# Kernel optimization log

Hardware: AMD Instinct MI355X
Metric: run time of the kernel (lower is better)

Reference implementation:

```python
import jax, jax.numpy as jnp
import numpy as np

K = 20000   # know_num
I = 50000   # item_num
D = 128     # emb_dim
N = K + I   # nodes in exer+know graphs (exercises first)
E1 = 320000 # edges in directed knowledge graph
E2 = 640000 # edges in each exer<->know graph


def setup_inputs() -> dict:
    key = jax.random.key(0)
    ks = jax.random.split(key, 20)
    s = 1.0 / np.sqrt(D)
    s2 = 1.0 / np.sqrt(2 * D)
    return {
        'kn_emb': jax.random.normal(ks[0], (K, D), jnp.float32),
        'exer_emb': jax.random.normal(ks[1], (I, D), jnp.float32),
        # GAT params: W is fc.weight.T ([in,out]); a is attn_fc.weight flattened ([2D])
        'W_dir': jax.random.normal(ks[2], (D, D), jnp.float32) * s,
        'a_dir': jax.random.normal(ks[3], (2 * D,), jnp.float32) * s2,
        'W_ke': jax.random.normal(ks[4], (D, D), jnp.float32) * s,
        'a_ke': jax.random.normal(ks[5], (2 * D,), jnp.float32) * s2,
        'W_ek': jax.random.normal(ks[6], (D, D), jnp.float32) * s,
        'a_ek': jax.random.normal(ks[7], (2 * D,), jnp.float32) * s2,
        # relation attention MLP: Linear(D,D)+bias, Tanh, Linear(D,1,no bias)
        'rel_W1': jax.random.normal(ks[8], (D, D), jnp.float32) * s,
        'rel_b1': jax.random.normal(ks[9], (D,), jnp.float32) * s,
        'rel_w2': jax.random.normal(ks[10], (D,), jnp.float32) * s,
        # edge lists (src, dst)
        'directed_src': jax.random.randint(ks[11], (E1,), 0, K),
        'directed_dst': jax.random.randint(ks[12], (E1,), 0, K),
        'ke_src': jax.random.randint(ks[13], (E2,), 0, N),
        'ke_dst': jax.random.randint(ks[14], (E2,), 0, N),
        'ek_src': jax.random.randint(ks[15], (E2,), 0, N),
        'ek_dst': jax.random.randint(ks[16], (E2,), 0, N),
    }


def _gat(h, W, a, src, dst, n):
    # GraphLayer: z = fc(h); e = leaky_relu(attn_fc([z_src; z_dst]));
    # alpha = softmax_e over dst; h_out = sum alpha * z_src
    z = h @ W                                   # [n_in, D]
    # split attn vector: cat([z_src,z_dst]) @ a == z_src@a[:D] + z_dst@a[D:]
    s_src = z @ a[:D]                           # [n_in]
    s_dst = z @ a[D:]                           # [n_in]
    e = jax.nn.leaky_relu(s_src[src] + s_dst[dst], 0.01)  # [E]
    m = jax.ops.segment_max(e, dst, num_segments=n)
    ex = jnp.exp(e - m[dst])
    den = jax.ops.segment_sum(ex, dst, num_segments=n)
    alpha = ex / den[dst]                       # segment softmax over in-edges
    return jax.ops.segment_sum(alpha[:, None] * z[src], dst, num_segments=n)


def reference(kn_emb, exer_emb, W_dir, a_dir, W_ke, a_ke, W_ek, a_ek,
              rel_W1, rel_b1, rel_w2,
              directed_src, directed_dst, ke_src, ke_dst, ek_src, ek_dst):
    A = _gat(kn_emb, W_dir, a_dir, directed_src, directed_dst, K)      # [K,D]
    ek = jnp.concatenate([exer_emb, kn_emb], axis=0)                   # [N,D]
    B = _gat(ek, W_ke, a_ke, ke_src, ke_dst, N)[I:]                    # [K,D]
    Cfull = _gat(ek, W_ek, a_ek, ek_src, ek_dst, N)                    # [N,D]
    s1 = jnp.tanh(A @ rel_W1 + rel_b1) @ rel_w2                        # [K]
    s2 = jnp.tanh(B @ rel_W1 + rel_b1) @ rel_w2                        # [K]
    score = jax.nn.softmax(jnp.stack([s1, s2], axis=1), axis=1)        # [K,2]
    kn_out = score[:, 0:1] * A + score[:, 1:2] * B                     # [K,D]
    exer_out = Cfull[:I]                                               # [I,D]
    return (kn_out, exer_out)
```

## Files before the change

### kernel.cpp

```cpp
#include <hip/hip_runtime.h>
#include <math.h>

#define KN   20000
#define IN_  50000
#define DD   128
#define NN   70000
#define E1N  320000
#define E2N  640000

#define GB0  313
#define GB1  1094
#define GB2  1094
#define GTILES 2501

#define GROUPS 313
#define MGRID  (GROUPS*13)
#define CNT_CHUNKS 1563

#define CAP   64
#define LCAP  6

typedef _Float16 f16x8 __attribute__((ext_vector_type(8)));
typedef float floatx4 __attribute__((ext_vector_type(4)));

__device__ __forceinline__ unsigned f2bf(float x) {
  unsigned u = __float_as_uint(x);
  return (u + 0x7FFFu + ((u >> 16) & 1u)) >> 16;
}
__device__ __forceinline__ unsigned packbf(float a, float b) {
  return f2bf(a) | (f2bf(b) << 16);
}
__device__ __forceinline__ float bf_lo(unsigned u) { return __uint_as_float(u << 16); }
__device__ __forceinline__ float bf_hi(unsigned u) { return __uint_as_float(u & 0xFFFF0000u); }

__device__ __forceinline__ float ftanh(float x) {
  x = fminf(15.f, fmaxf(-15.f, x));
  float t = __expf(2.f * x);
  return (t - 1.f) / (t + 1.f);
}

__global__ __launch_bounds__(256) void prep(
    const float* __restrict__ W0, const float* __restrict__ W1,
    const float* __restrict__ W2, const float* __restrict__ W3,
    short* __restrict__ wfr)
{
  int b = blockIdx.x;
  int wsel = b >> 3;
  const float* W = (wsel == 0) ? W0 : (wsel == 1) ? W1 : (wsel == 2) ? W2 : W3;
  int fi = (b & 7) * 256 + threadIdx.x;
  int l = fi & 63, chunk = (fi >> 6) & 3, t = fi >> 8;
  int col = t * 16 + (l & 15);
  int kbase = chunk * 32 + (l >> 4) * 8;
  f16x8 hv;
#pragma unroll
  for (int j = 0; j < 8; ++j) hv[j] = (_Float16)W[(kbase + j) * 128 + col];
  ((f16x8*)(wfr + wsel * 16384))[fi] = hv;
}

__global__ __launch_bounds__(256, 4) void gemm3_insert(
    const float* __restrict__ kn, const float* __restrict__ ex,
    const short* __restrict__ wfr,
    const float* __restrict__ a_dir, const float* __restrict__ a_ke, const float* __restrict__ a_ek,
    unsigned* __restrict__ zb_dir, unsigned* __restrict__ zb_ke, unsigned* __restrict__ zb_ek,
    float* __restrict__ sds, float* __restrict__ sdd,
    float* __restrict__ sks, float* __restrict__ skd,
    float* __restrict__ ses, float* __restrict__ sed,
    const int* __restrict__ dsrc, const int* __restrict__ ddst,
    const int* __restrict__ kesrc, const int* __restrict__ kedst,
    const int* __restrict__ eksrc, const int* __restrict__ ekdst,
    int* __restrict__ cur_dir, int* __restrict__ cur_ke, int* __restrict__ cur_ek,
    int* __restrict__ epp_dir, int* __restrict__ epp_ke, int* __restrict__ epp_ek)
{
  __shared__ short sW[16384];
  const int g = blockIdx.x / 13;
  const int r = blockIdx.x % 13;
  const int tid = threadIdx.x;

  if (r >= 8) {
    int cidx = g * 5 + (r - 8);
    if (cidx >= CNT_CHUNKS) return;
    int t = cidx * 256 + tid;
    if (t < 80000) {
      int e0 = t * 4;
      int4 s4 = *(const int4*)(dsrc + e0);
      int4 d4 = *(const int4*)(ddst + e0);
      int p;
      p = atomicAdd(&cur_dir[d4.x], 1); if (p < CAP) epp_dir[(d4.x << LCAP) + p] = s4.x;
      p = atomicAdd(&cur_dir[d4.y], 1); if (p < CAP) epp_dir[(d4.y << LCAP) + p] = s4.y;
      p = atomicAdd(&cur_dir[d4.z], 1); if (p < CAP) epp_dir[(d4.z << LCAP) + p] = s4.z;
      p = atomicAdd(&cur_dir[d4.w], 1); if (p < CAP) epp_dir[(d4.w << LCAP) + p] = s4.w;
    } else if (t < 240000) {
      int e0 = (t - 80000) * 4;
      int4 s4 = *(const int4*)(kesrc + e0);
      int4 d4 = *(const int4*)(kedst + e0);
      int p;
      if (d4.x >= IN_) { p = atomicAdd(&cur_ke[d4.x - IN_], 1); if (p < CAP) epp_ke[((d4.x - IN_) << LCAP) + p] = s4.x; }
      if (d4.y >= IN_) { p = atomicAdd(&cur_ke[d4.y - IN_], 1); if (p < CAP) epp_ke[((d4.y - IN_) << LCAP) + p] = s4.y; }
      if (d4.z >= IN_) { p = atomicAdd(&cur_ke[d4.z - IN_], 1); if (p < CAP) epp_ke[((d4.z - IN_) << LCAP) + p] = s4.z; }
      if (d4.w >= IN_) { p = atomicAdd(&cur_ke[d4.w - IN_], 1); if (p < CAP) epp_ke[((d4.w - IN_) << LCAP) + p] = s4.w; }
    } else if (t < 400000) {
      int e0 = (t - 240000) * 4;
      int4 s4 = *(const int4*)(eksrc + e0);
      int4 d4 = *(const int4*)(ekdst + e0);
      int p;
      if (d4.x < IN_) { p = atomicAdd(&cur_ek[d4.x], 1); if (p < CAP) epp_ek[(d4.x << LCAP) + p] = s4.x; }
      if (d4.y < IN_) { p = atomicAdd(&cur_ek[d4.y], 1); if (p < CAP) epp_ek[(d4.y << LCAP) + p] = s4.y; }
      if (d4.z < IN_) { p = atomicAdd(&cur_ek[d4.z], 1); if (p < CAP) epp_ek[(d4.z << LCAP) + p] = s4.z; }
      if (d4.w < IN_) { p = atomicAdd(&cur_ek[d4.w], 1); if (p < CAP) epp_ek[(d4.w << LCAP) + p] = s4.w; }
    }
    return;
  }

  const int bid = g * 8 + r;
  if (bid >= GTILES) return;

  const float *h1, *h2, *avec;
  unsigned* zb;
  float *ssrc, *sdst;
  const short* wf;
  int split, rows, tile;
  if (bid < GB0) {
    tile = bid; rows = KN; split = KN; h1 = kn; h2 = kn;
    wf = wfr; avec = a_dir; zb = zb_dir; ssrc = sds; sdst = sdd;
  } else if (bid < GB0 + GB1) {
    tile = bid - GB0; rows = NN; split = IN_; h1 = ex; h2 = kn;
    wf = wfr + 16384; avec = a_ke; zb = zb_ke; ssrc = sks; sdst = skd;
  } else {
    tile = bid - GB0 - GB1; rows = NN; split = IN_; h1 = ex; h2 = kn;
    wf = wfr + 32768; avec = a_ek; zb = zb_ek; ssrc = ses; sdst = sed;
  }

  {
    const int4* gs = (const int4*)wf;
    int4* ls = (int4*)sW;
#pragma unroll
    for (int it = 0; it < 8; ++it) ls[it * 256 + tid] = gs[it * 256 + tid];
  }
  __syncthreads();

  const int lane = tid & 63;
  const int wv = tid >> 6;
  const int q = lane >> 4;
  const int m = lane & 15;
  const int rr = tile * 64 + wv * 16 + m;
  const int rc = (rr < rows) ? rr : (rows - 1);
  const float* hp = (rc < split) ? (h1 + (size_t)rc * 128)
                                 : (h2 + (size_t)(rc - split) * 128);

  floatx4 acc[8];
#pragma unroll
  for (int t = 0; t < 8; ++t) { acc[t][0]=0.f; acc[t][1]=0.f; acc[t][2]=0.f; acc[t][3]=0.f; }

#pragma unroll
  for (int chunk = 0; chunk < 4; ++chunk) {
    float4 v0 = *(const float4*)(hp + chunk * 32 + q * 8);
    float4 v1 = *(const float4*)(hp + chunk * 32 + q * 8 + 4);
    float vs[8] = {v0.x, v0.y, v0.z, v0.w, v1.x, v1.y, v1.z, v1.w};
    f16x8 ahi, alo;
#pragma unroll
    for (int j = 0; j < 8; ++j) {
      _Float16 h = (_Float16)vs[j];
      ahi[j] = h;
      alo[j] = (_Float16)(vs[j] - (float)h);
    }
#pragma unroll
    for (int t = 0; t < 8; ++t) {
      f16x8 bh = ((const f16x8*)sW)[(t * 4 + chunk) * 64 + lane];
      acc[t] = __builtin_amdgcn_mfma_f32_16x16x32_f16(bh, ahi, acc[t], 0, 0, 0);
      acc[t] = __builtin_amdgcn_mfma_f32_16x16x32_f16(bh, alo, acc[t], 0, 0, 0);
    }
  }

  if (rr < rows) {
    unsigned* zrow = zb + (size_t)rr * 64;
#pragma unroll
    for (int t = 0; t < 8; ++t) {
      uint2 pk;
      pk.x = packbf(acc[t][0], acc[t][1]);
      pk.y = packbf(acc[t][2], acc[t][3]);
      *(uint2*)(zrow + t * 8 + q * 2) = pk;
    }
  }
  float d1 = 0.f, d2 = 0.f;
#pragma unroll
  for (int t = 0; t < 8; ++t) {
    float4 wa = *(const float4*)(avec + t * 16 + q * 4);
    float4 wb = *(const float4*)(avec + 128 + t * 16 + q * 4);
    d1 += acc[t][0] * wa.x + acc[t][1] * wa.y + acc[t][2] * wa.z + acc[t][3] * wa.w;
    d2 += acc[t][0] * wb.x + acc[t][1] * wb.y + acc[t][2] * wb.z + acc[t][3] * wb.w;
  }
  d1 += __shfl_xor(d1, 16, 64); d1 += __shfl_xor(d1, 32, 64);
  d2 += __shfl_xor(d2, 16, 64); d2 += __shfl_xor(d2, 32, 64);
  if (q == 0 && rr < rows) { ssrc[rr] = d1; sdst[rr] = d2; }
}

__global__ __launch_bounds__(256) void gat_gather(
    const int* __restrict__ cur_dir, const int* __restrict__ epp_dir,
    const float* __restrict__ sds, const float* __restrict__ sdd,
    const unsigned* __restrict__ zb_dir, float* __restrict__ A,
    const int* __restrict__ cur_ke, const int* __restrict__ epp_ke,
    const float* __restrict__ sks, const float* __restrict__ skd,
    const unsigned* __restrict__ zb_ke, float* __restrict__ Bm,
    const int* __restrict__ cur_ek, const int* __restrict__ epp_ek,
    const float* __restrict__ ses, const float* __restrict__ sed,
    const unsigned* __restrict__ zb_ek, float* __restrict__ Cout)
{
  int gw = (blockIdx.x * 256 + threadIdx.x) >> 6;
  int lane = threadIdx.x & 63;
  int h = lane >> 5;
  int ln31 = lane & 31;
  int gh = (lane >> 4) & 1;
  int gl = lane & 15;

  const int *cur, *ep;
  const float *ss, *sD;
  const unsigned* zb;
  float* out;
  int s0, nodeoff;
  if (gw < 10000)      { s0 = 2 * gw;           cur = cur_dir; ep = epp_dir; ss = sds; sD = sdd; zb = zb_dir; out = A;    nodeoff = 0; }
  else if (gw < 20000) { s0 = 2 * (gw - 10000); cur = cur_ke;  ep = epp_ke;  ss = sks; sD = skd; zb = zb_ke;  out = Bm;   nodeoff = IN_; }
  else                 { s0 = 2 * (gw - 20000); cur = cur_ek;  ep = epp_ek;  ss = ses; sD = sed; zb = zb_ek;  out = Cout; nodeoff = 0; }

  int2 cc = *(const int2*)(cur + s0);
  int cnt = h ? cc.y : cc.x;
  cnt = (cnt < CAP) ? cnt : CAP;
  int b = (s0 + h) << LCAP;
  float sd = sD[s0 + h + nodeoff];
  int lim = (cnt < 32) ? cnt : 32;

  int   src_l = 0;
  float w_l   = 0.f;
  if (ln31 < lim) {
    int s = ep[b + ln31];
    src_l = s;
    float x = ss[s] + sd;
    x = (x > 0.f) ? x : 0.01f * x;
    w_l = __expf(x);
  }

  float den = w_l;
  den += __shfl_xor(den, 1, 64);
  den += __shfl_xor(den, 2, 64);
  den += __shfl_xor(den, 4, 64);
  den += __shfl_xor(den, 8, 64);
  den += __shfl_xor(den, 16, 64);

  float av[8];
#pragma unroll
  for (int k = 0; k < 8; ++k) av[k] = 0.f;

  for (int j0 = 0; j0 < lim; j0 += 8) {
    int base = h * 32 + j0 + gh * 4;
    int   s1 = __shfl(src_l, base + 0, 64); float w1 = __shfl(w_l, base + 0, 64);
    int   s2 = __shfl(src_l, base + 1, 64); float w2 = __shfl(w_l, base + 1, 64);
    int   s3 = __shfl(src_l, base + 2, 64); float w3 = __shfl(w_l, base + 2, 64);
    int   s4 = __shfl(src_l, base + 3, 64); float w4 = __shfl(w_l, base + 3, 64);
    uint4 za = *(const uint4*)(zb + (size_t)s1 * 64 + gl * 4);
    uint4 zc = *(const uint4*)(zb + (size_t)s2 * 64 + gl * 4);
    uint4 ze = *(const uint4*)(zb + (size_t)s3 * 64 + gl * 4);
    uint4 zg = *(const uint4*)(zb + (size_t)s4 * 64 + gl * 4);
    av[0] += w1 * bf_lo(za.x); av[1] += w1 * bf_hi(za.x);
    av[2] += w1 * bf_lo(za.y); av[3] += w1 * bf_hi(za.y);
    av[4] += w1 * bf_lo(za.z); av[5] += w1 * bf_hi(za.z);
    av[6] += w1 * bf_lo(za.w); av[7] += w1 * bf_hi(za.w);
    av[0] += w2 * bf_lo(zc.x); av[1] += w2 * bf_hi(zc.x);
    av[2] += w2 * bf_lo(zc.y); av[3] += w2 * bf_hi(zc.y);
    av[4] += w2 * bf_lo(zc.z); av[5] += w2 * bf_hi(zc.z);
    av[6] += w2 * bf_lo(zc.w); av[7] += w2 * bf_hi(zc.w);
    av[0] += w3 * bf_lo(ze.x); av[1] += w3 * bf_hi(ze.x);
    av[2] += w3 * bf_lo(ze.y); av[3] += w3 * bf_hi(ze.y);
    av[4] += w3 * bf_lo(ze.z); av[5] += w3 * bf_hi(ze.z);
    av[6] += w3 * bf_lo(ze.w); av[7] += w3 * bf_hi(ze.w);
    av[0] += w4 * bf_lo(zg.x); av[1] += w4 * bf_hi(zg.x);
    av[2] += w4 * bf_lo(zg.y); av[3] += w4 * bf_hi(zg.y);
    av[4] += w4 * bf_lo(zg.z); av[5] += w4 * bf_hi(zg.z);
    av[6] += w4 * bf_lo(zg.w); av[7] += w4 * bf_hi(zg.w);
  }

  if (cnt > 32) {
    float dtail = 0.f;
    int e = b + cnt;
    for (int i = b + 32 + gh; i < e; i += 2) {
      int sx = ep[i];
      float x1 = ss[sx] + sd;
      x1 = (x1 > 0.f) ? x1 : 0.01f * x1;
      float w1 = __expf(x1);
      uint4 za = *(const uint4*)(zb + (size_t)sx * 64 + gl * 4);
      dtail += w1;
      av[0] += w1 * bf_lo(za.x); av[1] += w1 * bf_hi(za.x);
      av[2] += w1 * bf_lo(za.y); av[3] += w1 * bf_hi(za.y);
      av[4] += w1 * bf_lo(za.z); av[5] += w1 * bf_hi(za.z);
      av[6] += w1 * bf_lo(za.w); av[7] += w1 * bf_hi(za.w);
    }
    den += dtail + __shfl_xor(dtail, 16, 64);
  }

#pragma unroll
  for (int k = 0; k < 8; ++k) av[k] += __shfl_xor(av[k], 16, 64);

  if (cnt > 0) {
    float inv = 1.f / den;
#pragma unroll
    for (int k = 0; k < 8; ++k) av[k] *= inv;
  }

  if (gh == 0) {
    int seg = s0 + h;
    float* op = out + (size_t)seg * 128 + gl * 8;
    *(float4*)op       = make_float4(av[0], av[1], av[2], av[3]);
    *(float4*)(op + 4) = make_float4(av[4], av[5], av[6], av[7]);
  }
}

__global__ __launch_bounds__(256, 2) void relgemm_combine(
    const float* __restrict__ Am, const float* __restrict__ Bm,
    const short* __restrict__ wfr_rel,
    const float* __restrict__ rb1, const float* __restrict__ rw2,
    float* __restrict__ out)
{
  __shared__ short sW[16384];
  const int tid = threadIdx.x;
  {
    const int4* gs = (const int4*)wfr_rel;
    int4* ls = (int4*)sW;
#pragma unroll
    for (int it = 0; it < 8; ++it) ls[it * 256 + tid] = gs[it * 256 + tid];
  }
  __syncthreads();

  const int lane = tid & 63;
  const int wv = tid >> 6;
  const int q = lane >> 4;
  const int m = lane & 15;
  const int r = blockIdx.x * 64 + wv * 16 + m;
  const int rc = (r < KN) ? r : (KN - 1);
  const float* hA = Am + (size_t)rc * 128;
  const float* hB = Bm + (size_t)rc * 128;

  floatx4 accA[8], accB[8];
#pragma unroll
  for (int t = 0; t < 8; ++t) {
    accA[t][0]=0.f; accA[t][1]=0.f; accA[t][2]=0.f; accA[t][3]=0.f;
    accB[t][0]=0.f; accB[t][1]=0.f; accB[t][2]=0.f; accB[t][3]=0.f;
  }

#pragma unroll
  for (int chunk = 0; chunk < 4; ++chunk) {
    float4 a0 = *(const float4*)(hA + chunk * 32 + q * 8);
    float4 a1 = *(const float4*)(hA + chunk * 32 + q * 8 + 4);
    float4 b0 = *(const float4*)(hB + chunk * 32 + q * 8);
    float4 b1 = *(const float4*)(hB + chunk * 32 + q * 8 + 4);
    float as[8] = {a0.x, a0.y, a0.z, a0.w, a1.x, a1.y, a1.z, a1.w};
    float bs[8] = {b0.x, b0.y, b0.z, b0.w, b1.x, b1.y, b1.z, b1.w};
    f16x8 ahiA, aloA, ahiB, aloB;
#pragma unroll
    for (int j = 0; j < 8; ++j) {
      _Float16 ha = (_Float16)as[j];
      ahiA[j] = ha; aloA[j] = (_Float16)(as[j] - (float)ha);
      _Float16 hb = (_Float16)bs[j];
      ahiB[j] = hb; aloB[j] = (_Float16)(bs[j] - (float)hb);
    }
#pragma unroll
    for (int t = 0; t < 8; ++t) {
      f16x8 bh = ((const f16x8*)sW)[(t * 4 + chunk) * 64 + lane];
      accA[t] = __builtin_amdgcn_mfma_f32_16x16x32_f16(bh, ahiA, accA[t], 0, 0, 0);
      accA[t] = __builtin_amdgcn_mfma_f32_16x16x32_f16(bh, aloA, accA[t], 0, 0, 0);
      accB[t] = __builtin_amdgcn_mfma_f32_16x16x32_f16(bh, ahiB, accB[t], 0, 0, 0);
      accB[t] = __builtin_amdgcn_mfma_f32_16x16x32_f16(bh, aloB, accB[t], 0, 0, 0);
    }
  }

  float p1 = 0.f, p2 = 0.f;
#pragma unroll
  for (int t = 0; t < 8; ++t) {
    float4 bb = *(const float4*)(rb1 + t * 16 + q * 4);
    float4 ww = *(const float4*)(rw2 + t * 16 + q * 4);
    p1 += ftanh(accA[t][0] + bb.x) * ww.x + ftanh(accA[t][1] + bb.y) * ww.y +
          ftanh(accA[t][2] + bb.z) * ww.z + ftanh(accA[t][3] + bb.w) * ww.w;
    p2 += ftanh(accB[t][0] + bb.x) * ww.x + ftanh(accB[t][1] + bb.y) * ww.y +
          ftanh(accB[t][2] + bb.z) * ww.z + ftanh(accB[t][3] + bb.w) * ww.w;
  }
  p1 += __shfl_xor(p1, 16, 64); p1 += __shfl_xor(p1, 32, 64);
  p2 += __shfl_xor(p2, 16, 64); p2 += __shfl_xor(p2, 32, 64);

  float mx = fmaxf(p1, p2);
  float e1 = __expf(p1 - mx), e2 = __expf(p2 - mx);
  float al = e1 / (e1 + e2), be = e2 / (e1 + e2);

  if (r < KN) {
#pragma unroll
    for (int t = 0; t < 8; ++t) {
      int col = t * 16 + q * 4;
      float4 avv = *(const float4*)(Am + (size_t)r * 128 + col);
      float4 bvv = *(const float4*)(Bm + (size_t)r * 128 + col);
      *(float4*)(out + (size_t)r * 128 + col) =
          make_float4(al * avv.x + be * bvv.x, al * avv.y + be * bvv.y,
                      al * avv.z + be * bvv.z, al * avv.w + be * bvv.w);
    }
  }
}

extern "C" void kernel_launch(void* const* d_in, const int* in_sizes, int n_in,
                              void* d_out, int out_size, void* d_ws, size_t ws_size,
                              hipStream_t stream) {
  const float* kn    = (const float*)d_in[0];
  const float* ex    = (const float*)d_in[1];
  const float* W_dir = (const float*)d_in[2];
  const float* a_dir = (const float*)d_in[3];
  const float* W_ke  = (const float*)d_in[4];
  const float* a_ke  = (const float*)d_in[5];
  const float* W_ek  = (const float*)d_in[6];
  const float* a_ek  = (const float*)d_in[7];
  const float* rW1   = (const float*)d_in[8];
  const float* rb1   = (const float*)d_in[9];
  const float* rw2   = (const float*)d_in[10];
  const int* dsrc    = (const int*)d_in[11];
  const int* ddst    = (const int*)d_in[12];
  const int* kesrc   = (const int*)d_in[13];
  const int* kedst   = (const int*)d_in[14];
  const int* eksrc   = (const int*)d_in[15];
  const int* ekdst   = (const int*)d_in[16];
  float* out = (float*)d_out;

  char* p = (char*)d_ws;
  auto alloc = [&](size_t bytes) {
    char* r = p;
    p += (bytes + 255) & ~(size_t)255;
    return r;
  };
  unsigned* zb_dir = (unsigned*)alloc((size_t)KN * 64 * 4);
  unsigned* zb_ke  = (unsigned*)alloc((size_t)NN * 64 * 4);
  unsigned* zb_ek  = (unsigned*)alloc((size_t)NN * 64 * 4);
  float* Am    = (float*)alloc((size_t)KN * 128 * 4);
  float* Bmat  = (float*)alloc((size_t)KN * 128 * 4);
  short* wfr   = (short*)alloc((size_t)4 * 16384 * 2);
  float* sds = (float*)alloc(KN * 4);
  float* sdd = (float*)alloc(KN * 4);
  float* sks = (float*)alloc(NN * 4);
  float* skd = (float*)alloc(NN * 4);
  float* ses = (float*)alloc(NN * 4);
  float* sed = (float*)alloc(NN * 4);
  int* cur = (int*)alloc((size_t)(KN + KN + IN_) * 4);
  int* cur_dir = cur;
  int* cur_ke  = cur + KN;
  int* cur_ek  = cur + 2 * KN;
  int* epp_dir = (int*)alloc((size_t)KN * CAP * 4);
  int* epp_ke  = (int*)alloc((size_t)KN * CAP * 4);
  int* epp_ek  = (int*)alloc((size_t)IN_ * CAP * 4);

  hipMemsetAsync(cur, 0, (size_t)(KN + KN + IN_) * 4, stream);

  prep<<<32, 256, 0, stream>>>(W_dir, W_ke, W_ek, rW1, wfr);

  gemm3_insert<<<MGRID, 256, 0, stream>>>(
      kn, ex, wfr, a_dir, a_ke, a_ek,
      zb_dir, zb_ke, zb_ek,
      sds, sdd, sks, skd, ses, sed,
      dsrc, ddst, kesrc, kedst, eksrc, ekdst,
      cur_dir, cur_ke, cur_ek,
      epp_dir, epp_ke, epp_ek);

  gat_gather<<<11250, 256, 0, stream>>>(
      cur_dir, epp_dir, sds, sdd, zb_dir, Am,
      cur_ke,  epp_ke,  sks, skd, zb_ke,  Bmat,
      cur_ek,  epp_ek,  ses, sed, zb_ek,  out + (size_t)KN * 128);

  relgemm_combine<<<313, 256, 0, stream>>>(Am, Bmat, wfr + 3 * 16384, rb1, rw2, out);
}
```

Before: 231.1 us.

## Fuse ke/ek projection GEMMs per tile and drop weight prep kernel

Removes the separate prep kernel. Each block now converts the fp32 weight matrix to the fp16 MFMA fragment layout directly in shared memory. The ke and ek projections share the same input rows, so one block loads and splits each row tile into hi/lo fp16 once and runs both GEMMs. This halves input reads for those graphs and cuts a launch. The cost is strided fp32 weight loads and conversion repeated in every block. The grid interleaving with edge-insertion blocks is also rebalanced (9 GEMM + 10 count blocks per group).

```diff
diff --git a/kernel.cpp b/kernel.cpp
--- a/kernel.cpp
+++ b/kernel.cpp
@@ -10,11 +10,10 @@
 
 #define GB0  313
 #define GB1  1094
-#define GB2  1094
-#define GTILES 2501
-
-#define GROUPS 313
-#define MGRID  (GROUPS*13)
+#define GTILES 1407
+
+#define GROUPS 157
+#define MGRID  (GROUPS*19)
 #define CNT_CHUNKS 1563
 
 #define CAP   64
@@ -39,27 +38,24 @@
   return (t - 1.f) / (t + 1.f);
 }
 
-__global__ __launch_bounds__(256) void prep(
-    const float* __restrict__ W0, const float* __restrict__ W1,
-    const float* __restrict__ W2, const float* __restrict__ W3,
-    short* __restrict__ wfr)
-{
-  int b = blockIdx.x;
-  int wsel = b >> 3;
-  const float* W = (wsel == 0) ? W0 : (wsel == 1) ? W1 : (wsel == 2) ? W2 : W3;
-  int fi = (b & 7) * 256 + threadIdx.x;
-  int l = fi & 63, chunk = (fi >> 6) & 3, t = fi >> 8;
-  int col = t * 16 + (l & 15);
-  int kbase = chunk * 32 + (l >> 4) * 8;
-  f16x8 hv;
-#pragma unroll
-  for (int j = 0; j < 8; ++j) hv[j] = (_Float16)W[(kbase + j) * 128 + col];
-  ((f16x8*)(wfr + wsel * 16384))[fi] = hv;
+__device__ __forceinline__ void stage_w(const float* __restrict__ W,
+                                        short* __restrict__ sW, int tid) {
+#pragma unroll
+  for (int it = 0; it < 8; ++it) {
+    int fi = it * 256 + tid;
+    int l = fi & 63, chunk = (fi >> 6) & 3, t = fi >> 8;
+    int col = t * 16 + (l & 15);
+    int kbase = chunk * 32 + (l >> 4) * 8;
+    f16x8 hv;
+#pragma unroll
+    for (int j = 0; j < 8; ++j) hv[j] = (_Float16)W[(kbase + j) * 128 + col];
+    ((f16x8*)sW)[fi] = hv;
+  }
 }
 
 __global__ __launch_bounds__(256, 4) void gemm3_insert(
     const float* __restrict__ kn, const float* __restrict__ ex,
-    const short* __restrict__ wfr,
+    const float* __restrict__ W_dir, const float* __restrict__ W_ke, const float* __restrict__ W_ek,
     const float* __restrict__ a_dir, const float* __restrict__ a_ke, const float* __restrict__ a_ek,
     unsigned* __restrict__ zb_dir, unsigned* __restrict__ zb_ke, unsigned* __restrict__ zb_ek,
     float* __restrict__ sds, float* __restrict__ sdd,
@@ -72,12 +68,12 @@
     int* __restrict__ epp_dir, int* __restrict__ epp_ke, int* __restrict__ epp_ek)
 {
   __shared__ short sW[16384];
-  const int g = blockIdx.x / 13;
-  const int r = blockIdx.x % 13;
+  const int g = blockIdx.x / 19;
+  const int r = blockIdx.x % 19;
   const int tid = threadIdx.x;
 
-  if (r >= 8) {
-    int cidx = g * 5 + (r - 8);
+  if (r >= 9) {
+    int cidx = g * 10 + (r - 9);
     if (cidx >= CNT_CHUNKS) return;
     int t = cidx * 256 + tid;
     if (t < 80000) {
@@ -111,87 +107,169 @@
     return;
   }
 
-  const int bid = g * 8 + r;
+  const int bid = g * 9 + r;
   if (bid >= GTILES) return;
-
-  const float *h1, *h2, *avec;
-  unsigned* zb;
-  float *ssrc, *sdst;
-  const short* wf;
-  int split, rows, tile;
-  if (bid < GB0) {
-    tile = bid; rows = KN; split = KN; h1 = kn; h2 = kn;
-    wf = wfr; avec = a_dir; zb = zb_dir; ssrc = sds; sdst = sdd;
-  } else if (bid < GB0 + GB1) {
-    tile = bid - GB0; rows = NN; split = IN_; h1 = ex; h2 = kn;
-    wf = wfr + 16384; avec = a_ke; zb = zb_ke; ssrc = sks; sdst = skd;
-  } else {
-    tile = bid - GB0 - GB1; rows = NN; split = IN_; h1 = ex; h2 = kn;
-    wf = wfr + 32768; avec = a_ek; zb = zb_ek; ssrc = ses; sdst = sed;
-  }
-
-  {
-    const int4* gs = (const int4*)wf;
-    int4* ls = (int4*)sW;
-#pragma unroll
-    for (int it = 0; it < 8; ++it) ls[it * 256 + tid] = gs[it * 256 + tid];
-  }
-  __syncthreads();
 
   const int lane = tid & 63;
   const int wv = tid >> 6;
   const int q = lane >> 4;
   const int m = lane & 15;
-  const int rr = tile * 64 + wv * 16 + m;
-  const int rc = (rr < rows) ? rr : (rows - 1);
-  const float* hp = (rc < split) ? (h1 + (size_t)rc * 128)
-                                 : (h2 + (size_t)(rc - split) * 128);
-
-  floatx4 acc[8];
-#pragma unroll
-  for (int t = 0; t < 8; ++t) { acc[t][0]=0.f; acc[t][1]=0.f; acc[t][2]=0.f; acc[t][3]=0.f; }
-
-#pragma unroll
-  for (int chunk = 0; chunk < 4; ++chunk) {
-    float4 v0 = *(const float4*)(hp + chunk * 32 + q * 8);
-    float4 v1 = *(const float4*)(hp + chunk * 32 + q * 8 + 4);
-    float vs[8] = {v0.x, v0.y, v0.z, v0.w, v1.x, v1.y, v1.z, v1.w};
-    f16x8 ahi, alo;
-#pragma unroll
-    for (int j = 0; j < 8; ++j) {
-      _Float16 h = (_Float16)vs[j];
-      ahi[j] = h;
-      alo[j] = (_Float16)(vs[j] - (float)h);
-    }
+
+  if (bid < GB0) {
+    const int rr = bid * 64 + wv * 16 + m;
+    const int rc = (rr < KN) ? rr : (KN - 1);
+    const float* hp = kn + (size_t)rc * 128;
+
+    stage_w(W_dir, sW, tid);
+    __syncthreads();
+
+    floatx4 acc[8];
+#pragma unroll
+    for (int t = 0; t < 8; ++t) { acc[t][0]=0.f; acc[t][1]=0.f; acc[t][2]=0.f; acc[t][3]=0.f; }
+
+#pragma unroll
+    for (int chunk = 0; chunk < 4; ++chunk) {
+      float4 v0 = *(const float4*)(hp + chunk * 32 + q * 8);
+      float4 v1 = *(const float4*)(hp + chunk * 32 + q * 8 + 4);
+      float vs[8] = {v0.x, v0.y, v0.z, v0.w, v1.x, v1.y, v1.z, v1.w};
+      f16x8 ahi, alo;
+#pragma unroll
+      for (int j = 0; j < 8; ++j) {
+        _Float16 h = (_Float16)vs[j];
+        ahi[j] = h;
+        alo[j] = (_Float16)(vs[j] - (float)h);
+      }
+#pragma unroll
+      for (int t = 0; t < 8; ++t) {
+        f16x8 bh = ((const f16x8*)sW)[(t * 4 + chunk) * 64 + lane];
+        acc[t] = __builtin_amdgcn_mfma_f32_16x16x32_f16(bh, ahi, acc[t], 0, 0, 0);
+        acc[t] = __builtin_amdgcn_mfma_f32_16x16x32_f16(bh, alo, acc[t], 0, 0, 0);
+      }
+    }
+
+    if (rr < KN) {
+      unsigned* zrow = zb_dir + (size_t)rr * 64;
+#pragma unroll
+      for (int t = 0; t < 8; ++t) {
+        uint2 pk;
+        pk.x = packbf(acc[t][0], acc[t][1]);
+        pk.y = packbf(acc[t][2], acc[t][3]);
+        *(uint2*)(zrow + t * 8 + q * 2) = pk;
+      }
+    }
+    float d1 = 0.f, d2 = 0.f;
 #pragma unroll
     for (int t = 0; t < 8; ++t) {
-      f16x8 bh = ((const f16x8*)sW)[(t * 4 + chunk) * 64 + lane];
-      acc[t] = __builtin_amdgcn_mfma_f32_16x16x32_f16(bh, ahi, acc[t], 0, 0, 0);
-      acc[t] = __builtin_amdgcn_mfma_f32_16x16x32_f16(bh, alo, acc[t], 0, 0, 0);
-    }
-  }
-
-  if (rr < rows) {
-    unsigned* zrow = zb + (size_t)rr * 64;
-#pragma unroll
-    for (int t = 0; t < 8; ++t) {
-      uint2 pk;
-      pk.x = packbf(acc[t][0], acc[t][1]);
-      pk.y = packbf(acc[t][2], acc[t][3]);
-      *(uint2*)(zrow + t * 8 + q * 2) = pk;
-    }
-  }
-  float d1 = 0.f, d2 = 0.f;
-#pragma unroll
-  for (int t = 0; t < 8; ++t) {
-    float4 wa = *(const float4*)(avec + t * 16 + q * 4);
-    float4 wb = *(const float4*)(avec + 128 + t * 16 + q * 4);
-    d1 += acc[t][0] * wa.x + acc[t][1] * wa.y + acc[t][2] * wa.z + acc[t][3] * wa.w;
-    d2 += acc[t][0] * wb.x + acc[t][1] * wb.y + acc[t][2] * wb.z + acc[t][3] * wb.w;
-  }
-  d1 += __shfl_xor(d1, 16, 64); d1 += __shfl_xor(d1, 32, 64);
-  d2 += __shfl_xor(d2, 16, 64); d2 += __shfl_xor(d2, 32, 64);
-  if (q == 0 && rr < rows) { ssrc[rr] = d1; sdst[rr] = d2; }
+      float4 wa = *(const float4*)(a_dir + t * 16 + q * 4);
+      float4 wb = *(const float4*)(a_dir + 128 + t * 16 + q * 4);
+      d1 += acc[t][0] * wa.x + acc[t][1] * wa.y + acc[t][2] * wa.z + acc[t][3] * wa.w;
+      d2 += acc[t][0] * wb.x + acc[t][1] * wb.y + acc[t][2] * wb.z + acc[t][3] * wb.w;
+    }
+    d1 += __shfl_xor(d1, 16, 64); d1 += __shfl_xor(d1, 32, 64);
+    d2 += __shfl_xor(d2, 16, 64); d2 += __shfl_xor(d2, 32, 64);
+    if (q == 0 && rr < KN) { sds[rr] = d1; sdd[rr] = d2; }
+    return;
+  }
+
+  {
+    const int tile = bid - GB0;
+    const int rr = tile * 64 + wv * 16 + m;
+    const int rc = (rr < NN) ? rr : (NN - 1);
+    const float* hp = (rc < IN_) ? (ex + (size_t)rc * 128)
+                                 : (kn + (size_t)(rc - IN_) * 128);
+
+    f16x8 fhi[4], flo[4];
+#pragma unroll
+    for (int chunk = 0; chunk < 4; ++chunk) {
+      float4 v0 = *(const float4*)(hp + chunk * 32 + q * 8);
+      float4 v1 = *(const float4*)(hp + chunk * 32 + q * 8 + 4);
+      float vs[8] = {v0.x, v0.y, v0.z, v0.w, v1.x, v1.y, v1.z, v1.w};
+#pragma unroll
+      for (int j = 0; j < 8; ++j) {
+        _Float16 h = (_Float16)vs[j];
+        fhi[chunk][j] = h;
+        flo[chunk][j] = (_Float16)(vs[j] - (float)h);
+      }
+    }
+
+    stage_w(W_ke, sW, tid);
+    __syncthreads();
+
+    floatx4 acc[8];
+#pragma unroll
+    for (int t = 0; t < 8; ++t) { acc[t][0]=0.f; acc[t][1]=0.f; acc[t][2]=0.f; acc[t][3]=0.f; }
+#pragma unroll
+    for (int chunk = 0; chunk < 4; ++chunk) {
+#pragma unroll
+      for (int t = 0; t < 8; ++t) {
+        f16x8 bh = ((const f16x8*)sW)[(t * 4 + chunk) * 64 + lane];
+        acc[t] = __builtin_amdgcn_mfma_f32_16x16x32_f16(bh, fhi[chunk], acc[t], 0, 0, 0);
+        acc[t] = __builtin_amdgcn_mfma_f32_16x16x32_f16(bh, flo[chunk], acc[t], 0, 0, 0);
+      }
+    }
+    if (rr < NN) {
+      unsigned* zrow = zb_ke + (size_t)rr * 64;
+#pragma unroll
+      for (int t = 0; t < 8; ++t) {
+        uint2 pk;
+        pk.x = packbf(acc[t][0], acc[t][1]);
+        pk.y = packbf(acc[t][2], acc[t][3]);
+        *(uint2*)(zrow + t * 8 + q * 2) = pk;
+      }
+    }
+    {
+      float d1 = 0.f, d2 = 0.f;
+#pragma unroll
+      for (int t = 0; t < 8; ++t) {
+        float4 wa = *(const float4*)(a_ke + t * 16 + q * 4);
+        float4 wb = *(const float4*)(a_ke + 128 + t * 16 + q * 4);
+        d1 += acc[t][0] * wa.x + acc[t][1] * wa.y + acc[t][2] * wa.z + acc[t][3] * wa.w;
+        d2 += acc[t][0] * wb.x + acc[t][1] * wb.y + acc[t][2] * wb.z + acc[t][3] * wb.w;
+      }
+      d1 += __shfl_xor(d1, 16, 64); d1 += __shfl_xor(d1, 32, 64);
+      d2 += __shfl_xor(d2, 16, 64); d2 += __shfl_xor(d2, 32, 64);
+      if (q == 0 && rr < NN) { sks[rr] = d1; skd[rr] = d2; }
+    }
+
+    __syncthreads();
+    stage_w(W_ek, sW, tid);
+    __syncthreads();
+
+#pragma unroll
+    for (int t = 0; t < 8; ++t) { acc[t][0]=0.f; acc[t][1]=0.f; acc[t][2]=0.f; acc[t][3]=0.f; }
+#pragma unroll
+    for (int chunk = 0; chunk < 4; ++chunk) {
+#pragma unroll
+      for (int t = 0; t < 8; ++t) {
+        f16x8 bh = ((const f16x8*)sW)[(t * 4 + chunk) * 64 + lane];
+        acc[t] = __builtin_amdgcn_mfma_f32_16x16x32_f16(bh, fhi[chunk], acc[t], 0, 0, 0);
+        acc[t] = __builtin_amdgcn_mfma_f32_16x16x32_f16(bh, flo[chunk], acc[t], 0, 0, 0);
+      }
+    }
+    if (rr < NN) {
+      unsigned* zrow = zb_ek + (size_t)rr * 64;
+#pragma unroll
+      for (int t = 0; t < 8; ++t) {
+        uint2 pk;
+        pk.x = packbf(acc[t][0], acc[t][1]);
+        pk.y = packbf(acc[t][2], acc[t][3]);
+        *(uint2*)(zrow + t * 8 + q * 2) = pk;
+      }
+    }
+    {
+      float d1 = 0.f, d2 = 0.f;
+#pragma unroll
+      for (int t = 0; t < 8; ++t) {
+        float4 wa = *(const float4*)(a_ek + t * 16 + q * 4);
+        float4 wb = *(const float4*)(a_ek + 128 + t * 16 + q * 4);
+        d1 += acc[t][0] * wa.x + acc[t][1] * wa.y + acc[t][2] * wa.z + acc[t][3] * wa.w;
+        d2 += acc[t][0] * wb.x + acc[t][1] * wb.y + acc[t][2] * wb.z + acc[t][3] * wb.w;
+      }
+      d1 += __shfl_xor(d1, 16, 64); d1 += __shfl_xor(d1, 32, 64);
+      d2 += __shfl_xor(d2, 16, 64); d2 += __shfl_xor(d2, 32, 64);
+      if (q == 0 && rr < NN) { ses[rr] = d1; sed[rr] = d2; }
+    }
+  }
 }
 
 __global__ __launch_bounds__(256) void gat_gather(
@@ -314,18 +392,13 @@
 
 __global__ __launch_bounds__(256, 2) void relgemm_combine(
     const float* __restrict__ Am, const float* __restrict__ Bm,
-    const short* __restrict__ wfr_rel,
+    const float* __restrict__ rW1,
     const float* __restrict__ rb1, const float* __restrict__ rw2,
     float* __restrict__ out)
 {
   __shared__ short sW[16384];
   const int tid = threadIdx.x;
-  {
-    const int4* gs = (const int4*)wfr_rel;
-    int4* ls = (int4*)sW;
-#pragma unroll
-    for (int it = 0; it < 8; ++it) ls[it * 256 + tid] = gs[it * 256 + tid];
-  }
+  stage_w(rW1, sW, tid);
   __syncthreads();
 
   const int lane = tid & 63;
@@ -433,7 +506,6 @@
   unsigned* zb_ek  = (unsigned*)alloc((size_t)NN * 64 * 4);
   float* Am    = (float*)alloc((size_t)KN * 128 * 4);
   float* Bmat  = (float*)alloc((size_t)KN * 128 * 4);
-  short* wfr   = (short*)alloc((size_t)4 * 16384 * 2);
   float* sds = (float*)alloc(KN * 4);
   float* sdd = (float*)alloc(KN * 4);
   float* sks = (float*)alloc(NN * 4);
@@ -450,10 +522,8 @@
 
   hipMemsetAsync(cur, 0, (size_t)(KN + KN + IN_) * 4, stream);
 
-  prep<<<32, 256, 0, stream>>>(W_dir, W_ke, W_ek, rW1, wfr);
-
   gemm3_insert<<<MGRID, 256, 0, stream>>>(
-      kn, ex, wfr, a_dir, a_ke, a_ek,
+      kn, ex, W_dir, W_ke, W_ek, a_dir, a_ke, a_ek,
       zb_dir, zb_ke, zb_ek,
       sds, sdd, sks, skd, ses, sed,
       dsrc, ddst, kesrc, kedst, eksrc, ekdst,
@@ -465,5 +535,5 @@
       cur_ke,  epp_ke,  sks, skd, zb_ke,  Bmat,
       cur_ek,  epp_ek,  ses, sed, zb_ek,  out + (size_t)KN * 128);
 
-  relgemm_combine<<<313, 256, 0, stream>>>(Am, Bmat, wfr + 3 * 16384, rb1, rw2, out);
-}
+  relgemm_combine<<<313, 256, 0, stream>>>(Am, Bmat, rW1, rb1, rw2, out);
+}
```

New measurement: 236.0 us. 1.02x slower.

## Fuse weight prep and edge bucketing into every GEMM block

Applied to the files above, without the earlier changes.

Removes the separate prep kernel. Each GEMM block now converts its fp32 weight matrix into the fp16 fragment layout directly in shared memory, and relgemm_combine does the same for the relation weight. Edge bucket insertion moves from dedicated blocks into every GEMM block: each block claims bucket slots with atomics before the MFMA work and writes the edge sources after it, so atomic latency overlaps compute. The three bucket arrays are merged into one buffer. The cost is redundant strided weight conversion in every one of the 2501 blocks and extra registers held across the GEMM.

```diff
diff --git a/kernel.cpp b/kernel.cpp
--- a/kernel.cpp
+++ b/kernel.cpp
@@ -7,18 +7,17 @@
 #define NN   70000
 #define E1N  320000
 #define E2N  640000
+#define ETOT 1600000
 
 #define GB0  313
 #define GB1  1094
-#define GB2  1094
 #define GTILES 2501
 
-#define GROUPS 313
-#define MGRID  (GROUPS*13)
-#define CNT_CHUNKS 1563
+#define EPB  768
 
 #define CAP   64
 #define LCAP  6
+#define NSEG  90000
 
 typedef _Float16 f16x8 __attribute__((ext_vector_type(8)));
 typedef float floatx4 __attribute__((ext_vector_type(4)));
@@ -39,27 +38,24 @@
   return (t - 1.f) / (t + 1.f);
 }
 
-__global__ __launch_bounds__(256) void prep(
-    const float* __restrict__ W0, const float* __restrict__ W1,
-    const float* __restrict__ W2, const float* __restrict__ W3,
-    short* __restrict__ wfr)
-{
-  int b = blockIdx.x;
-  int wsel = b >> 3;
-  const float* W = (wsel == 0) ? W0 : (wsel == 1) ? W1 : (wsel == 2) ? W2 : W3;
-  int fi = (b & 7) * 256 + threadIdx.x;
-  int l = fi & 63, chunk = (fi >> 6) & 3, t = fi >> 8;
-  int col = t * 16 + (l & 15);
-  int kbase = chunk * 32 + (l >> 4) * 8;
-  f16x8 hv;
-#pragma unroll
-  for (int j = 0; j < 8; ++j) hv[j] = (_Float16)W[(kbase + j) * 128 + col];
-  ((f16x8*)(wfr + wsel * 16384))[fi] = hv;
-}
-
-__global__ __launch_bounds__(256, 4) void gemm3_insert(
+__device__ __forceinline__ void stage_w(const float* __restrict__ W,
+                                        short* __restrict__ sW, int tid) {
+#pragma unroll
+  for (int it = 0; it < 8; ++it) {
+    int fi = it * 256 + tid;
+    int l = fi & 63, chunk = (fi >> 6) & 3, t = fi >> 8;
+    int col = t * 16 + (l & 15);
+    int kbase = chunk * 32 + (l >> 4) * 8;
+    f16x8 hv;
+#pragma unroll
+    for (int j = 0; j < 8; ++j) hv[j] = (_Float16)W[(kbase + j) * 128 + col];
+    ((f16x8*)sW)[fi] = hv;
+  }
+}
+
+__global__ __launch_bounds__(256, 4) void gemm3i(
     const float* __restrict__ kn, const float* __restrict__ ex,
-    const short* __restrict__ wfr,
+    const float* __restrict__ W_dir, const float* __restrict__ W_ke, const float* __restrict__ W_ek,
     const float* __restrict__ a_dir, const float* __restrict__ a_ke, const float* __restrict__ a_ek,
     unsigned* __restrict__ zb_dir, unsigned* __restrict__ zb_ke, unsigned* __restrict__ zb_ek,
     float* __restrict__ sds, float* __restrict__ sdd,
@@ -68,75 +64,55 @@
     const int* __restrict__ dsrc, const int* __restrict__ ddst,
     const int* __restrict__ kesrc, const int* __restrict__ kedst,
     const int* __restrict__ eksrc, const int* __restrict__ ekdst,
-    int* __restrict__ cur_dir, int* __restrict__ cur_ke, int* __restrict__ cur_ek,
-    int* __restrict__ epp_dir, int* __restrict__ epp_ke, int* __restrict__ epp_ek)
+    int* __restrict__ cur, int* __restrict__ epp)
 {
   __shared__ short sW[16384];
-  const int g = blockIdx.x / 13;
-  const int r = blockIdx.x % 13;
+  const int bid = blockIdx.x;
   const int tid = threadIdx.x;
 
-  if (r >= 8) {
-    int cidx = g * 5 + (r - 8);
-    if (cidx >= CNT_CHUNKS) return;
-    int t = cidx * 256 + tid;
-    if (t < 80000) {
-      int e0 = t * 4;
-      int4 s4 = *(const int4*)(dsrc + e0);
-      int4 d4 = *(const int4*)(ddst + e0);
-      int p;
-      p = atomicAdd(&cur_dir[d4.x], 1); if (p < CAP) epp_dir[(d4.x << LCAP) + p] = s4.x;
-      p = atomicAdd(&cur_dir[d4.y], 1); if (p < CAP) epp_dir[(d4.y << LCAP) + p] = s4.y;
-      p = atomicAdd(&cur_dir[d4.z], 1); if (p < CAP) epp_dir[(d4.z << LCAP) + p] = s4.z;
-      p = atomicAdd(&cur_dir[d4.w], 1); if (p < CAP) epp_dir[(d4.w << LCAP) + p] = s4.w;
-    } else if (t < 240000) {
-      int e0 = (t - 80000) * 4;
-      int4 s4 = *(const int4*)(kesrc + e0);
-      int4 d4 = *(const int4*)(kedst + e0);
-      int p;
-      if (d4.x >= IN_) { p = atomicAdd(&cur_ke[d4.x - IN_], 1); if (p < CAP) epp_ke[((d4.x - IN_) << LCAP) + p] = s4.x; }
-      if (d4.y >= IN_) { p = atomicAdd(&cur_ke[d4.y - IN_], 1); if (p < CAP) epp_ke[((d4.y - IN_) << LCAP) + p] = s4.y; }
-      if (d4.z >= IN_) { p = atomicAdd(&cur_ke[d4.z - IN_], 1); if (p < CAP) epp_ke[((d4.z - IN_) << LCAP) + p] = s4.z; }
-      if (d4.w >= IN_) { p = atomicAdd(&cur_ke[d4.w - IN_], 1); if (p < CAP) epp_ke[((d4.w - IN_) << LCAP) + p] = s4.w; }
-    } else if (t < 400000) {
-      int e0 = (t - 240000) * 4;
-      int4 s4 = *(const int4*)(eksrc + e0);
-      int4 d4 = *(const int4*)(ekdst + e0);
-      int p;
-      if (d4.x < IN_) { p = atomicAdd(&cur_ek[d4.x], 1); if (p < CAP) epp_ek[(d4.x << LCAP) + p] = s4.x; }
-      if (d4.y < IN_) { p = atomicAdd(&cur_ek[d4.y], 1); if (p < CAP) epp_ek[(d4.y << LCAP) + p] = s4.y; }
-      if (d4.z < IN_) { p = atomicAdd(&cur_ek[d4.z], 1); if (p < CAP) epp_ek[(d4.z << LCAP) + p] = s4.z; }
-      if (d4.w < IN_) { p = atomicAdd(&cur_ek[d4.w], 1); if (p < CAP) epp_ek[(d4.w << LCAP) + p] = s4.w; }
-    }
-    return;
-  }
-
-  const int bid = g * 8 + r;
-  if (bid >= GTILES) return;
-
-  const float *h1, *h2, *avec;
+  const float *h1, *h2, *avec, *W;
   unsigned* zb;
   float *ssrc, *sdst;
-  const short* wf;
   int split, rows, tile;
   if (bid < GB0) {
     tile = bid; rows = KN; split = KN; h1 = kn; h2 = kn;
-    wf = wfr; avec = a_dir; zb = zb_dir; ssrc = sds; sdst = sdd;
+    W = W_dir; avec = a_dir; zb = zb_dir; ssrc = sds; sdst = sdd;
   } else if (bid < GB0 + GB1) {
     tile = bid - GB0; rows = NN; split = IN_; h1 = ex; h2 = kn;
-    wf = wfr + 16384; avec = a_ke; zb = zb_ke; ssrc = sks; sdst = skd;
+    W = W_ke; avec = a_ke; zb = zb_ke; ssrc = sks; sdst = skd;
   } else {
     tile = bid - GB0 - GB1; rows = NN; split = IN_; h1 = ex; h2 = kn;
-    wf = wfr + 32768; avec = a_ek; zb = zb_ek; ssrc = ses; sdst = sed;
-  }
-
+    W = W_ek; avec = a_ek; zb = zb_ek; ssrc = ses; sdst = sed;
+  }
+
+  stage_w(W, sW, tid);
+  __syncthreads();
+
+  int ci[3], sv[3], pp[3];
   {
-    const int4* gs = (const int4*)wf;
-    int4* ls = (int4*)sW;
-#pragma unroll
-    for (int it = 0; it < 8; ++it) ls[it * 256 + tid] = gs[it * 256 + tid];
-  }
-  __syncthreads();
+    const int ebase = bid * EPB + tid;
+#pragma unroll
+    for (int k = 0; k < 3; ++k) {
+      int e = ebase + k * 256;
+      int c = -1, s = 0;
+      if (e < E1N) {
+        s = dsrc[e];
+        c = ddst[e];
+      } else if (e < E1N + E2N) {
+        int i = e - E1N;
+        s = kesrc[i];
+        int d = kedst[i];
+        c = (d >= IN_) ? (20000 + d - IN_) : -1;
+      } else if (e < ETOT) {
+        int i = e - E1N - E2N;
+        s = eksrc[i];
+        int d = ekdst[i];
+        c = (d < IN_) ? (40000 + d) : -1;
+      }
+      ci[k] = c; sv[k] = s;
+      pp[k] = (c >= 0) ? atomicAdd(&cur[c], 1) : 0;
+    }
+  }
 
   const int lane = tid & 63;
   const int wv = tid >> 6;
@@ -192,6 +168,11 @@
   d1 += __shfl_xor(d1, 16, 64); d1 += __shfl_xor(d1, 32, 64);
   d2 += __shfl_xor(d2, 16, 64); d2 += __shfl_xor(d2, 32, 64);
   if (q == 0 && rr < rows) { ssrc[rr] = d1; sdst[rr] = d2; }
+
+#pragma unroll
+  for (int k = 0; k < 3; ++k) {
+    if (ci[k] >= 0 && pp[k] < CAP) epp[(ci[k] << LCAP) + pp[k]] = sv[k];
+  }
 }
 
 __global__ __launch_bounds__(256) void gat_gather(
@@ -314,18 +295,13 @@
 
 __global__ __launch_bounds__(256, 2) void relgemm_combine(
     const float* __restrict__ Am, const float* __restrict__ Bm,
-    const short* __restrict__ wfr_rel,
+    const float* __restrict__ rW1,
     const float* __restrict__ rb1, const float* __restrict__ rw2,
     float* __restrict__ out)
 {
   __shared__ short sW[16384];
   const int tid = threadIdx.x;
-  {
-    const int4* gs = (const int4*)wfr_rel;
-    int4* ls = (int4*)sW;
-#pragma unroll
-    for (int it = 0; it < 8; ++it) ls[it * 256 + tid] = gs[it * 256 + tid];
-  }
+  stage_w(rW1, sW, tid);
   __syncthreads();
 
   const int lane = tid & 63;
@@ -433,37 +409,28 @@
   unsigned* zb_ek  = (unsigned*)alloc((size_t)NN * 64 * 4);
   float* Am    = (float*)alloc((size_t)KN * 128 * 4);
   float* Bmat  = (float*)alloc((size_t)KN * 128 * 4);
-  short* wfr   = (short*)alloc((size_t)4 * 16384 * 2);
   float* sds = (float*)alloc(KN * 4);
   float* sdd = (float*)alloc(KN * 4);
   float* sks = (float*)alloc(NN * 4);
   float* skd = (float*)alloc(NN * 4);
   float* ses = (float*)alloc(NN * 4);
   float* sed = (float*)alloc(NN * 4);
-  int* cur = (int*)alloc((size_t)(KN + KN + IN_) * 4);
-  int* cur_dir = cur;
-  int* cur_ke  = cur + KN;
-  int* cur_ek  = cur + 2 * KN;
-  int* epp_dir = (int*)alloc((size_t)KN * CAP * 4);
-  int* epp_ke  = (int*)alloc((size_t)KN * CAP * 4);
-  int* epp_ek  = (int*)alloc((size_t)IN_ * CAP * 4);
-
-  hipMemsetAsync(cur, 0, (size_t)(KN + KN + IN_) * 4, stream);
-
-  prep<<<32, 256, 0, stream>>>(W_dir, W_ke, W_ek, rW1, wfr);
-
-  gemm3_insert<<<MGRID, 256, 0, stream>>>(
-      kn, ex, wfr, a_dir, a_ke, a_ek,
+  int* cur = (int*)alloc((size_t)NSEG * 4);
+  int* epp = (int*)alloc((size_t)NSEG * CAP * 4);
+
+  hipMemsetAsync(cur, 0, (size_t)NSEG * 4, stream);
+
+  gemm3i<<<GTILES, 256, 0, stream>>>(
+      kn, ex, W_dir, W_ke, W_ek, a_dir, a_ke, a_ek,
       zb_dir, zb_ke, zb_ek,
       sds, sdd, sks, skd, ses, sed,
       dsrc, ddst, kesrc, kedst, eksrc, ekdst,
-      cur_dir, cur_ke, cur_ek,
-      epp_dir, epp_ke, epp_ek);
+      cur, epp);
 
   gat_gather<<<11250, 256, 0, stream>>>(
-      cur_dir, epp_dir, sds, sdd, zb_dir, Am,
-      cur_ke,  epp_ke,  sks, skd, zb_ke,  Bmat,
-      cur_ek,  epp_ek,  ses, sed, zb_ek,  out + (size_t)KN * 128);
-
-  relgemm_combine<<<313, 256, 0, stream>>>(Am, Bmat, wfr + 3 * 16384, rb1, rw2, out);
-}
+      cur,          epp,              sds, sdd, zb_dir, Am,
+      cur + 20000,  epp + 20000 * CAP, sks, skd, zb_ke,  Bmat,
+      cur + 40000,  epp + 40000 * CAP, ses, sed, zb_ek,  out + (size_t)KN * 128);
+
+  relgemm_combine<<<313, 256, 0, stream>>>(Am, Bmat, rW1, rb1, rw2, out);
+}
```

After: 243.7 us. 1.05x slower.
